# Kernel tuning notes

Hardware: AMD Instinct MI355X
Metric: run time of the kernel (lower is better)

The kernel has to match this reference:

```python
import jax, jax.numpy as jnp
import numpy as np

B, N, C, H, NC = 8, 4096, 512, 256, 1000
GRID = 64  # N = GRID*GRID unique positions
LN_EPS = 1e-5


def setup_inputs() -> dict:
    key = jax.random.key(0)
    ks = jax.random.split(key, 10)
    # unique integer grid positions, same for every batch element (original order)
    i = jnp.arange(N)
    base = jnp.stack([i % GRID, i // GRID], axis=-1).astype(jnp.float32)  # [N,2]
    pos_org = jnp.broadcast_to(base, (B, N, 2))
    # per-batch random permutation -> shuffled positions (as the backbone would emit)
    perm = jax.vmap(lambda k: jax.random.permutation(k, N))(jax.random.split(ks[0], B))  # [B,N]
    pos_shuffled = jnp.take_along_axis(pos_org, perm[..., None], axis=1)
    s = 0.02
    return {
        "feat": jax.random.normal(ks[1], (B, N, C), jnp.float32),
        "prev_out": jax.random.normal(ks[2], (B, N, C), jnp.float32),
        "pos_org": pos_org,
        "pos_shuffled": pos_shuffled,
        "proj_W": jax.random.normal(ks[3], (C, C), jnp.float32) * s,
        "proj_b": jnp.zeros((C,), jnp.float32),
        "ln_g": jnp.ones((C,), jnp.float32),
        "ln_b": jnp.zeros((C,), jnp.float32),
        "W1": jax.random.normal(ks[4], (H, C), jnp.float32) * s,
        "b1": jnp.zeros((H,), jnp.float32),
        "W2": jax.random.normal(ks[5], (H, H), jnp.float32) * s,
        "b2": jnp.zeros((H,), jnp.float32),
        "W3": jax.random.normal(ks[6], (NC, H), jnp.float32) * s,
        "b3": jnp.zeros((NC,), jnp.float32),
    }


def _layernorm(x, g, b):
    x32 = x.astype(jnp.float32)
    mu = x32.mean(-1, keepdims=True)
    var = ((x32 - mu) ** 2).mean(-1, keepdims=True)
    return (x32 - mu) * jax.lax.rsqrt(var + LN_EPS) * g + b


def reference(feat, prev_out, pos_org, pos_shuffled, proj_W, proj_b,
              ln_g, ln_b, W1, b1, W2, b2, W3, b3):
    # find_pos_org_order: L1 cdist [B,N,N] + argmin over shuffled axis
    dists = jnp.abs(pos_org[:, :, None, :] - pos_shuffled[:, None, :, :]).sum(-1)
    pos_indices = jnp.argmin(dists, axis=2)  # [B,N]
    # batched gather: feat[b_, pos_indices]
    g = jnp.take_along_axis(feat, pos_indices[..., None], axis=1)  # [B,N,C]
    # fused proj -> layernorm (in fp32) -> cast back -> residual add
    proj = jnp.einsum('bnc,dc->bnd', g, proj_W) + proj_b
    out_feat = prev_out + _layernorm(proj, ln_g, ln_b).astype(feat.dtype)
    # mean-pool over tokens, 3-layer MLP head with relu on first two layers
    pooled = out_feat.mean(1)  # [B,C]
    h = jax.nn.relu(pooled @ W1.T + b1)
    h = jax.nn.relu(h @ W2.T + b2)
    return h @ W3.T + b3  # [B, num_classes]
```

## Files before the change

kernel.cpp:

```cpp
#include <hip/hip_runtime.h>
#include <stdint.h>

#define B_ 8
#define N_ 4096
#define C_ 512
#define H_ 256
#define NC_ 1000

typedef float v4f __attribute__((ext_vector_type(4)));
typedef short v8s __attribute__((ext_vector_type(8)));
typedef unsigned short ushort_t;

__device__ __forceinline__ uint32_t f2bf1(float f) {
    uint32_t u = __float_as_uint(f);
    return (u + 0x7FFFu + ((u >> 16) & 1u)) >> 16;
}
__device__ __forceinline__ uint32_t pk2(float lo, float hi) {
#if __has_builtin(__builtin_amdgcn_cvt_pk_bf16_f32)
    auto r = __builtin_amdgcn_cvt_pk_bf16_f32(lo, hi);
    return __builtin_bit_cast(uint32_t, r);
#else
    return f2bf1(lo) | (f2bf1(hi) << 16);
#endif
}

__global__ void prep_kernel(const float* __restrict__ W, ushort_t* __restrict__ Wfrag) {
    int i = blockIdx.x * 256 + threadIdx.x;
    int d = i >> 6, kb = (i >> 2) & 15, q = i & 3;
    const float4* src = (const float4*)(W + d * C_ + kb * 32 + q * 8);
    float4 v0 = src[0], v1 = src[1];
    uint4 pk;
    pk.x = pk2(v0.x, v0.y); pk.y = pk2(v0.z, v0.w);
    pk.z = pk2(v1.x, v1.y); pk.w = pk2(v1.z, v1.w);
    ((uint4*)Wfrag)[((d >> 4) * 16 + kb) * 64 + q * 16 + (d & 15)] = pk;
}

__device__ __forceinline__ void kstep(int kb, v4f (&acc)[4][4],
                                      const ushort_t* const (&fb)[4],
                                      const v8s* __restrict__ Abuf,
                                      int c, int q) {
    v8s af[4], bf[4];
#pragma unroll
    for (int nt = 0; nt < 4; nt++)
        bf[nt] = *((const v8s*)(fb[nt] + kb * 512));
#pragma unroll
    for (int mt = 0; mt < 4; mt++)
        af[mt] = Abuf[(mt * 16 + c) * 64 + ((kb * 4 + q) ^ (c & 7))];
#pragma unroll
    for (int mt = 0; mt < 4; mt++)
#pragma unroll
        for (int nt = 0; nt < 4; nt++)
            acc[mt][nt] = __builtin_amdgcn_mfma_f32_16x16x32_bf16(
                af[mt], bf[nt], acc[mt][nt], 0, 0, 0);
}

__global__ __launch_bounds__(512, 4)
void gemm_ln_pool(const float* __restrict__ feat, const float* __restrict__ prev,
                  const ushort_t* __restrict__ Wfrag,
                  const float* __restrict__ pb, const float* __restrict__ lg,
                  const float* __restrict__ lb,
                  float* __restrict__ partialG,
                  float* __restrict__ partialP) {
    __shared__ v8s Abuf[4096];
    __shared__ float RowS[64], RowQ[64];

    const int bid = blockIdx.x;
    const int t = threadIdx.x;

    if (bid % 3 == 2) {
        const int p = bid / 3;
        const int b = p >> 5;
        const int r0 = (p & 31) << 7;
        const int col4 = t & 127, rg = t >> 7;
        const v4f* psrc =
            (const v4f*)(prev + (size_t)(b * N_ + r0 + rg * 32) * C_) + col4;
        v4f a0 = {0.f, 0.f, 0.f, 0.f}, a1 = a0, a2 = a0, a3 = a0;
#pragma unroll
        for (int batch = 0; batch < 4; batch++) {
            v4f v[8];
#pragma unroll
            for (int j = 0; j < 8; j++)
                v[j] = __builtin_nontemporal_load(psrc + (batch * 8 + j) * 128);
            a0 += v[0]; a1 += v[1]; a2 += v[2]; a3 += v[3];
            a0 += v[4]; a1 += v[5]; a2 += v[6]; a3 += v[7];
        }
        v4f s = (a0 + a1) + (a2 + a3);
        float* AbufF = (float*)Abuf;
        ((v4f*)AbufF)[rg * 128 + col4] = s;
        __syncthreads();
        partialP[(size_t)p * 512 + t] =
            (AbufF[t] + AbufF[512 + t]) + (AbufF[1024 + t] + AbufF[1536 + t]);
        return;
    }

    const int gix = (bid / 3) * 2 + (bid % 3);
    const int b = gix >> 6;
    const int row0 = (gix & 63) << 6;
    const int wv = t >> 6, lane = t & 63, c = lane & 15, q = lane >> 4;

    if (t < 64) { RowS[t] = 0.f; RowQ[t] = 0.f; }

    const int arow = t >> 3;
    const int acol8 = t & 7;
    const v4f* asrc = (const v4f*)(feat + ((size_t)(b * N_ + row0 + arow) * C_));
#pragma unroll 2
    for (int s = 0; s < 4; s++) {
        const int chunk = s * 8 + acol8;
        v4f f0 = __builtin_nontemporal_load(asrc + chunk * 2);
        v4f f1 = __builtin_nontemporal_load(asrc + chunk * 2 + 1);
        uint4 pk;
        pk.x = pk2(f0.x, f0.y); pk.y = pk2(f0.z, f0.w);
        pk.z = pk2(f1.x, f1.y); pk.w = pk2(f1.z, f1.w);
        ((uint4*)Abuf)[arow * 64 + (chunk ^ (arow & 7))] = pk;
    }

    const ushort_t* fb[4];
#pragma unroll
    for (int nt = 0; nt < 4; nt++)
        fb[nt] = Wfrag + (wv * 4 + nt) * 8192 + lane * 8;

    v4f acc[4][4];
    const v4f vzero = {0.f, 0.f, 0.f, 0.f};
#pragma unroll
    for (int mt = 0; mt < 4; mt++)
#pragma unroll
        for (int nt = 0; nt < 4; nt++) acc[mt][nt] = vzero;

    __syncthreads();

#pragma unroll 2
    for (int kb = 0; kb < 6; kb++) kstep(kb, acc, fb, Abuf, c, q);

#pragma unroll 2
    for (int s = 4; s < 8; s++) {
        const int chunk = s * 8 + acol8;
        v4f f0 = __builtin_nontemporal_load(asrc + chunk * 2);
        v4f f1 = __builtin_nontemporal_load(asrc + chunk * 2 + 1);
        uint4 pk;
        pk.x = pk2(f0.x, f0.y); pk.y = pk2(f0.z, f0.w);
        pk.z = pk2(f1.x, f1.y); pk.w = pk2(f1.z, f1.w);
        ((uint4*)Abuf)[arow * 64 + (chunk ^ (arow & 7))] = pk;
    }

    kstep(6, acc, fb, Abuf, c, q);
    kstep(7, acc, fb, Abuf, c, q);
    __syncthreads();

#pragma unroll 2
    for (int kb = 8; kb < 16; kb++) kstep(kb, acc, fb, Abuf, c, q);

    float pb4[4], lg4[4], lb4[4];
#pragma unroll
    for (int nt = 0; nt < 4; nt++) {
        int n = wv * 64 + nt * 16 + c;
        pb4[nt] = pb[n]; lg4[nt] = lg[n]; lb4[nt] = lb[n];
    }
#pragma unroll
    for (int mt = 0; mt < 4; mt++) {
#pragma unroll
        for (int reg = 0; reg < 4; reg++) {
            float s1 = 0.f, s2 = 0.f;
#pragma unroll
            for (int nt = 0; nt < 4; nt++) {
                float v = acc[mt][nt][reg] + pb4[nt];
                acc[mt][nt][reg] = v;
                s1 += v; s2 += v * v;
            }
#pragma unroll
            for (int d = 1; d < 16; d <<= 1) {
                s1 += __shfl_xor(s1, d);
                s2 += __shfl_xor(s2, d);
            }
            if (c == 0) {
                int r = mt * 16 + q * 4 + reg;
                atomicAdd(&RowS[r], s1);
                atomicAdd(&RowQ[r], s2);
            }
        }
    }
    __syncthreads();
    if (t < 64) {
        float mu = RowS[t] * (1.f / C_);
        float var = RowQ[t] * (1.f / C_) - mu * mu;
        RowS[t] = mu;
        RowQ[t] = rsqrtf(var + 1e-5f);
    }
    __syncthreads();
    float col[4] = {0.f, 0.f, 0.f, 0.f};
#pragma unroll
    for (int mt = 0; mt < 4; mt++) {
#pragma unroll
        for (int reg = 0; reg < 4; reg++) {
            int r = mt * 16 + q * 4 + reg;
            float mu = RowS[r], rs = RowQ[r];
#pragma unroll
            for (int nt = 0; nt < 4; nt++)
                col[nt] += (acc[mt][nt][reg] - mu) * rs * lg4[nt] + lb4[nt];
        }
    }
#pragma unroll
    for (int nt = 0; nt < 4; nt++) {
        col[nt] += __shfl_xor(col[nt], 16);
        col[nt] += __shfl_xor(col[nt], 32);
    }
    if (lane < 16) {
#pragma unroll
        for (int nt = 0; nt < 4; nt++)
            partialG[(size_t)gix * 512 + wv * 64 + nt * 16 + c] = col[nt];
    }
}

__global__ __launch_bounds__(256)
void head_kernel(const float* __restrict__ partialG,
                 const float* __restrict__ partialP,
                 const float* __restrict__ W1, const float* __restrict__ b1,
                 const float* __restrict__ W2, const float* __restrict__ b2,
                 const float* __restrict__ W3, const float* __restrict__ b3,
                 float* __restrict__ out) {
    __shared__ __align__(16) float P[512];
    __shared__ __align__(16) float H1[256];
    __shared__ __align__(16) float H2[256];
    const int t = threadIdx.x, wv = t >> 6, lane = t & 63;
    const int b = blockIdx.x / 25;
    const int slice = blockIdx.x % 25;

    {
        const float* pg = partialG + (size_t)b * 64 * 512;
        const float* pp = partialP + (size_t)b * 32 * 512;
        float a0 = 0.f, a1 = 0.f, a2 = 0.f, a3 = 0.f;
#pragma unroll 4
        for (int i = 0; i < 64; i += 2) {
            a0 += pg[i * 512 + t];
            a1 += pg[(i + 1) * 512 + t];
            a2 += pg[i * 512 + t + 256];
            a3 += pg[(i + 1) * 512 + t + 256];
        }
#pragma unroll 4
        for (int i = 0; i < 32; i += 2) {
            a0 += pp[i * 512 + t];
            a1 += pp[(i + 1) * 512 + t];
            a2 += pp[i * 512 + t + 256];
            a3 += pp[(i + 1) * 512 + t + 256];
        }
        P[t] = (a0 + a1) * (1.f / 4096.f);
        P[t + 256] = (a2 + a3) * (1.f / 4096.f);
    }
    __syncthreads();

    {
        const float4* wr = (const float4*)(W1 + t * C_);
        float s = 0.f;
#pragma unroll 8
        for (int k = 0; k < 128; k++) {
            float4 w = wr[k];
            float4 p = ((const float4*)P)[k];
            s += w.x * p.x + w.y * p.y + w.z * p.z + w.w * p.w;
        }
        H1[t] = fmaxf(s + b1[t], 0.f);
    }
    __syncthreads();

    {
        const float4* wr = (const float4*)(W2 + t * H_);
        float s = 0.f;
#pragma unroll 8
        for (int k = 0; k < 64; k++) {
            float4 w = wr[k];
            float4 p = ((const float4*)H1)[k];
            s += w.x * p.x + w.y * p.y + w.z * p.z + w.w * p.w;
        }
        H2[t] = fmaxf(s + b2[t], 0.f);
    }
    __syncthreads();

#pragma unroll
    for (int jj = 0; jj < 10; jj++) {
        const int o = slice * 40 + jj * 4 + wv;
        float4 w = ((const float4*)(W3 + o * H_))[lane];
        float4 p = ((const float4*)H2)[lane];
        float s = w.x * p.x + w.y * p.y + w.z * p.z + w.w * p.w;
#pragma unroll
        for (int d = 1; d < 64; d <<= 1) s += __shfl_xor(s, d);
        if (lane == 0) out[b * NC_ + o] = s + b3[o];
    }
}

extern "C" void kernel_launch(void* const* d_in, const int* in_sizes, int n_in,
                              void* d_out, int out_size, void* d_ws, size_t ws_size,
                              hipStream_t stream) {
    const float* feat  = (const float*)d_in[0];
    const float* prev  = (const float*)d_in[1];
    const float* projW = (const float*)d_in[4];
    const float* pb    = (const float*)d_in[5];
    const float* lg    = (const float*)d_in[6];
    const float* lb    = (const float*)d_in[7];
    const float* W1    = (const float*)d_in[8];
    const float* b1    = (const float*)d_in[9];
    const float* W2    = (const float*)d_in[10];
    const float* b2    = (const float*)d_in[11];
    const float* W3    = (const float*)d_in[12];
    const float* b3    = (const float*)d_in[13];
    float* out = (float*)d_out;

    char* ws = (char*)d_ws;
    ushort_t* Wfrag  = (ushort_t*)ws;
    float* partialG  = (float*)(ws + 524288);
    float* partialP  = (float*)(ws + 1572864);

    prep_kernel<<<128, 256, 0, stream>>>(projW, Wfrag);
    gemm_ln_pool<<<768, 512, 0, stream>>>(feat, prev, Wfrag,
                                          pb, lg, lb, partialG, partialP);
    head_kernel<<<200, 256, 0, stream>>>(partialG, partialP,
                                         W1, b1, W2, b2, W3, b3, out);
}
```

Measured before the change: 222.3 us.

## Fuse MLP head into GEMM kernel via last-block-per-batch atomic counter

Drops the separate head kernel launch. Each block of the GEMM/pool kernel bumps a per-batch atomic counter after writing its partials, and the last of the 96 blocks for that batch reduces the partials and runs the three-layer MLP. This removes a kernel launch and its gap, but the head now runs on only 8 blocks instead of 200. Each thread also computes a whole 256-long W3 row serially, which could lengthen the tail.

```diff
diff --git a/kernel.cpp b/kernel.cpp
--- a/kernel.cpp
+++ b/kernel.cpp
@@ -24,8 +24,11 @@
 #endif
 }
 
-__global__ void prep_kernel(const float* __restrict__ W, ushort_t* __restrict__ Wfrag) {
-    int i = blockIdx.x * 256 + threadIdx.x;
+__global__ void prep_kernel(const float* __restrict__ W, ushort_t* __restrict__ Wfrag,
+                            uint32_t* __restrict__ counters) {
+    int t = threadIdx.x;
+    if (blockIdx.x == 0 && t < 8) counters[t] = 0;
+    int i = blockIdx.x * 256 + t;
     int d = i >> 6, kb = (i >> 2) & 15, q = i & 3;
     const float4* src = (const float4*)(W + d * C_ + kb * 32 + q * 8);
     float4 v0 = src[0], v1 = src[1];
@@ -60,16 +63,23 @@
                   const float* __restrict__ pb, const float* __restrict__ lg,
                   const float* __restrict__ lb,
                   float* __restrict__ partialG,
-                  float* __restrict__ partialP) {
+                  float* __restrict__ partialP,
+                  uint32_t* __restrict__ counters,
+                  const float* __restrict__ W1, const float* __restrict__ b1,
+                  const float* __restrict__ W2, const float* __restrict__ b2,
+                  const float* __restrict__ W3, const float* __restrict__ b3,
+                  float* __restrict__ out) {
     __shared__ v8s Abuf[4096];
     __shared__ float RowS[64], RowQ[64];
+    __shared__ int isLast;
 
     const int bid = blockIdx.x;
     const int t = threadIdx.x;
+    int b;
 
     if (bid % 3 == 2) {
         const int p = bid / 3;
-        const int b = p >> 5;
+        b = p >> 5;
         const int r0 = (p & 31) << 7;
         const int col4 = t & 127, rg = t >> 7;
         const v4f* psrc =
@@ -90,198 +100,196 @@
         __syncthreads();
         partialP[(size_t)p * 512 + t] =
             (AbufF[t] + AbufF[512 + t]) + (AbufF[1024 + t] + AbufF[1536 + t]);
-        return;
-    }
-
-    const int gix = (bid / 3) * 2 + (bid % 3);
-    const int b = gix >> 6;
-    const int row0 = (gix & 63) << 6;
-    const int wv = t >> 6, lane = t & 63, c = lane & 15, q = lane >> 4;
-
-    if (t < 64) { RowS[t] = 0.f; RowQ[t] = 0.f; }
-
-    const int arow = t >> 3;
-    const int acol8 = t & 7;
-    const v4f* asrc = (const v4f*)(feat + ((size_t)(b * N_ + row0 + arow) * C_));
+    } else {
+        const int gix = (bid / 3) * 2 + (bid % 3);
+        b = gix >> 6;
+        const int row0 = (gix & 63) << 6;
+        const int wv = t >> 6, lane = t & 63, c = lane & 15, q = lane >> 4;
+
+        if (t < 64) { RowS[t] = 0.f; RowQ[t] = 0.f; }
+
+        const int arow = t >> 3;
+        const int acol8 = t & 7;
+        const v4f* asrc = (const v4f*)(feat + ((size_t)(b * N_ + row0 + arow) * C_));
 #pragma unroll 2
-    for (int s = 0; s < 4; s++) {
-        const int chunk = s * 8 + acol8;
-        v4f f0 = __builtin_nontemporal_load(asrc + chunk * 2);
-        v4f f1 = __builtin_nontemporal_load(asrc + chunk * 2 + 1);
-        uint4 pk;
-        pk.x = pk2(f0.x, f0.y); pk.y = pk2(f0.z, f0.w);
-        pk.z = pk2(f1.x, f1.y); pk.w = pk2(f1.z, f1.w);
-        ((uint4*)Abuf)[arow * 64 + (chunk ^ (arow & 7))] = pk;
-    }
-
-    const ushort_t* fb[4];
-#pragma unroll
-    for (int nt = 0; nt < 4; nt++)
-        fb[nt] = Wfrag + (wv * 4 + nt) * 8192 + lane * 8;
-
-    v4f acc[4][4];
-    const v4f vzero = {0.f, 0.f, 0.f, 0.f};
-#pragma unroll
-    for (int mt = 0; mt < 4; mt++)
-#pragma unroll
-        for (int nt = 0; nt < 4; nt++) acc[mt][nt] = vzero;
-
-    __syncthreads();
+        for (int s = 0; s < 4; s++) {
+            const int chunk = s * 8 + acol8;
+            v4f f0 = __builtin_nontemporal_load(asrc + chunk * 2);
+            v4f f1 = __builtin_nontemporal_load(asrc + chunk * 2 + 1);
+            uint4 pk;
+            pk.x = pk2(f0.x, f0.y); pk.y = pk2(f0.z, f0.w);
+            pk.z = pk2(f1.x, f1.y); pk.w = pk2(f1.z, f1.w);
+            ((uint4*)Abuf)[arow * 64 + (chunk ^ (arow & 7))] = pk;
+        }
+
+        const ushort_t* fb[4];
+#pragma unroll
+        for (int nt = 0; nt < 4; nt++)
+            fb[nt] = Wfrag + (wv * 4 + nt) * 8192 + lane * 8;
+
+        v4f acc[4][4];
+        const v4f vzero = {0.f, 0.f, 0.f, 0.f};
+#pragma unroll
+        for (int mt = 0; mt < 4; mt++)
+#pragma unroll
+            for (int nt = 0; nt < 4; nt++) acc[mt][nt] = vzero;
+
+        __syncthreads();
 
 #pragma unroll 2
-    for (int kb = 0; kb < 6; kb++) kstep(kb, acc, fb, Abuf, c, q);
+        for (int kb = 0; kb < 6; kb++) kstep(kb, acc, fb, Abuf, c, q);
 
 #pragma unroll 2
-    for (int s = 4; s < 8; s++) {
-        const int chunk = s * 8 + acol8;
-        v4f f0 = __builtin_nontemporal_load(asrc + chunk * 2);
-        v4f f1 = __builtin_nontemporal_load(asrc + chunk * 2 + 1);
-        uint4 pk;
-        pk.x = pk2(f0.x, f0.y); pk.y = pk2(f0.z, f0.w);
-        pk.z = pk2(f1.x, f1.y); pk.w = pk2(f1.z, f1.w);
-        ((uint4*)Abuf)[arow * 64 + (chunk ^ (arow & 7))] = pk;
-    }
-
-    kstep(6, acc, fb, Abuf, c, q);
-    kstep(7, acc, fb, Abuf, c, q);
-    __syncthreads();
+        for (int s = 4; s < 8; s++) {
+            const int chunk = s * 8 + acol8;
+            v4f f0 = __builtin_nontemporal_load(asrc + chunk * 2);
+            v4f f1 = __builtin_nontemporal_load(asrc + chunk * 2 + 1);
+            uint4 pk;
+            pk.x = pk2(f0.x, f0.y); pk.y = pk2(f0.z, f0.w);
+            pk.z = pk2(f1.x, f1.y); pk.w = pk2(f1.z, f1.w);
+            ((uint4*)Abuf)[arow * 64 + (chunk ^ (arow & 7))] = pk;
+        }
+
+        kstep(6, acc, fb, Abuf, c, q);
+        kstep(7, acc, fb, Abuf, c, q);
+        __syncthreads();
 
 #pragma unroll 2
-    for (int kb = 8; kb < 16; kb++) kstep(kb, acc, fb, Abuf, c, q);
-
-    float pb4[4], lg4[4], lb4[4];
-#pragma unroll
-    for (int nt = 0; nt < 4; nt++) {
-        int n = wv * 64 + nt * 16 + c;
-        pb4[nt] = pb[n]; lg4[nt] = lg[n]; lb4[nt] = lb[n];
-    }
-#pragma unroll
-    for (int mt = 0; mt < 4; mt++) {
-#pragma unroll
-        for (int reg = 0; reg < 4; reg++) {
-            float s1 = 0.f, s2 = 0.f;
-#pragma unroll
-            for (int nt = 0; nt < 4; nt++) {
-                float v = acc[mt][nt][reg] + pb4[nt];
-                acc[mt][nt][reg] = v;
-                s1 += v; s2 += v * v;
+        for (int kb = 8; kb < 16; kb++) kstep(kb, acc, fb, Abuf, c, q);
+
+        float pb4[4], lg4[4], lb4[4];
+#pragma unroll
+        for (int nt = 0; nt < 4; nt++) {
+            int n = wv * 64 + nt * 16 + c;
+            pb4[nt] = pb[n]; lg4[nt] = lg[n]; lb4[nt] = lb[n];
+        }
+#pragma unroll
+        for (int mt = 0; mt < 4; mt++) {
+#pragma unroll
+            for (int reg = 0; reg < 4; reg++) {
+                float s1 = 0.f, s2 = 0.f;
+#pragma unroll
+                for (int nt = 0; nt < 4; nt++) {
+                    float v = acc[mt][nt][reg] + pb4[nt];
+                    acc[mt][nt][reg] = v;
+                    s1 += v; s2 += v * v;
+                }
+#pragma unroll
+                for (int d = 1; d < 16; d <<= 1) {
+                    s1 += __shfl_xor(s1, d);
+                    s2 += __shfl_xor(s2, d);
+                }
+                if (c == 0) {
+                    int r = mt * 16 + q * 4 + reg;
+                    atomicAdd(&RowS[r], s1);
+                    atomicAdd(&RowQ[r], s2);
+                }
             }
-#pragma unroll
-            for (int d = 1; d < 16; d <<= 1) {
-                s1 += __shfl_xor(s1, d);
-                s2 += __shfl_xor(s2, d);
+        }
+        __syncthreads();
+        if (t < 64) {
+            float mu = RowS[t] * (1.f / C_);
+            float var = RowQ[t] * (1.f / C_) - mu * mu;
+            RowS[t] = mu;
+            RowQ[t] = rsqrtf(var + 1e-5f);
+        }
+        __syncthreads();
+        float col[4] = {0.f, 0.f, 0.f, 0.f};
+#pragma unroll
+        for (int mt = 0; mt < 4; mt++) {
+#pragma unroll
+            for (int reg = 0; reg < 4; reg++) {
+                int r = mt * 16 + q * 4 + reg;
+                float mu = RowS[r], rs = RowQ[r];
+#pragma unroll
+                for (int nt = 0; nt < 4; nt++)
+                    col[nt] += (acc[mt][nt][reg] - mu) * rs * lg4[nt] + lb4[nt];
             }
-            if (c == 0) {
-                int r = mt * 16 + q * 4 + reg;
-                atomicAdd(&RowS[r], s1);
-                atomicAdd(&RowQ[r], s2);
-            }
-        }
-    }
-    __syncthreads();
-    if (t < 64) {
-        float mu = RowS[t] * (1.f / C_);
-        float var = RowQ[t] * (1.f / C_) - mu * mu;
-        RowS[t] = mu;
-        RowQ[t] = rsqrtf(var + 1e-5f);
-    }
-    __syncthreads();
-    float col[4] = {0.f, 0.f, 0.f, 0.f};
-#pragma unroll
-    for (int mt = 0; mt < 4; mt++) {
-#pragma unroll
-        for (int reg = 0; reg < 4; reg++) {
-            int r = mt * 16 + q * 4 + reg;
-            float mu = RowS[r], rs = RowQ[r];
+        }
+#pragma unroll
+        for (int nt = 0; nt < 4; nt++) {
+            col[nt] += __shfl_xor(col[nt], 16);
+            col[nt] += __shfl_xor(col[nt], 32);
+        }
+        if (lane < 16) {
 #pragma unroll
             for (int nt = 0; nt < 4; nt++)
-                col[nt] += (acc[mt][nt][reg] - mu) * rs * lg4[nt] + lb4[nt];
-        }
-    }
-#pragma unroll
-    for (int nt = 0; nt < 4; nt++) {
-        col[nt] += __shfl_xor(col[nt], 16);
-        col[nt] += __shfl_xor(col[nt], 32);
-    }
-    if (lane < 16) {
-#pragma unroll
-        for (int nt = 0; nt < 4; nt++)
-            partialG[(size_t)gix * 512 + wv * 64 + nt * 16 + c] = col[nt];
-    }
-}
-
-__global__ __launch_bounds__(256)
-void head_kernel(const float* __restrict__ partialG,
-                 const float* __restrict__ partialP,
-                 const float* __restrict__ W1, const float* __restrict__ b1,
-                 const float* __restrict__ W2, const float* __restrict__ b2,
-                 const float* __restrict__ W3, const float* __restrict__ b3,
-                 float* __restrict__ out) {
-    __shared__ __align__(16) float P[512];
-    __shared__ __align__(16) float H1[256];
-    __shared__ __align__(16) float H2[256];
-    const int t = threadIdx.x, wv = t >> 6, lane = t & 63;
-    const int b = blockIdx.x / 25;
-    const int slice = blockIdx.x % 25;
-
+                partialG[(size_t)gix * 512 + wv * 64 + nt * 16 + c] = col[nt];
+        }
+    }
+
+    __threadfence();
+    __syncthreads();
+    if (t == 0) {
+        uint32_t prev_cnt = atomicAdd(&counters[b], 1u);
+        isLast = (prev_cnt == 95u);
+    }
+    __syncthreads();
+    if (!isLast) return;
+    __threadfence();
+
+    float* P  = (float*)Abuf;
+    float* H1 = P + 512;
+    float* H2 = H1 + 256;
     {
-        const float* pg = partialG + (size_t)b * 64 * 512;
-        const float* pp = partialP + (size_t)b * 32 * 512;
+        const float* pg = partialG + (size_t)b * 64 * 512 + t;
+        const float* pp = partialP + (size_t)b * 32 * 512 + t;
         float a0 = 0.f, a1 = 0.f, a2 = 0.f, a3 = 0.f;
 #pragma unroll 4
-        for (int i = 0; i < 64; i += 2) {
-            a0 += pg[i * 512 + t];
-            a1 += pg[(i + 1) * 512 + t];
-            a2 += pg[i * 512 + t + 256];
-            a3 += pg[(i + 1) * 512 + t + 256];
+        for (int i = 0; i < 64; i += 4) {
+            a0 += pg[(i + 0) * 512]; a1 += pg[(i + 1) * 512];
+            a2 += pg[(i + 2) * 512]; a3 += pg[(i + 3) * 512];
         }
 #pragma unroll 4
-        for (int i = 0; i < 32; i += 2) {
-            a0 += pp[i * 512 + t];
-            a1 += pp[(i + 1) * 512 + t];
-            a2 += pp[i * 512 + t + 256];
-            a3 += pp[(i + 1) * 512 + t + 256];
-        }
-        P[t] = (a0 + a1) * (1.f / 4096.f);
-        P[t + 256] = (a2 + a3) * (1.f / 4096.f);
+        for (int i = 0; i < 32; i += 4) {
+            a0 += pp[(i + 0) * 512]; a1 += pp[(i + 1) * 512];
+            a2 += pp[(i + 2) * 512]; a3 += pp[(i + 3) * 512];
+        }
+        P[t] = ((a0 + a1) + (a2 + a3)) * (1.f / 4096.f);
     }
     __syncthreads();
 
     {
-        const float4* wr = (const float4*)(W1 + t * C_);
         float s = 0.f;
+        if (t < 256) {
+            const float4* wr = (const float4*)(W1 + t * C_);
 #pragma unroll 8
-        for (int k = 0; k < 128; k++) {
-            float4 w = wr[k];
-            float4 p = ((const float4*)P)[k];
-            s += w.x * p.x + w.y * p.y + w.z * p.z + w.w * p.w;
-        }
-        H1[t] = fmaxf(s + b1[t], 0.f);
+            for (int k = 0; k < 128; k++) {
+                float4 w = wr[k];
+                float4 p = ((const float4*)P)[k];
+                s += w.x * p.x + w.y * p.y + w.z * p.z + w.w * p.w;
+            }
+        }
+        __syncthreads();
+        if (t < 256) H1[t] = fmaxf(s + b1[t], 0.f);
     }
     __syncthreads();
 
     {
-        const float4* wr = (const float4*)(W2 + t * H_);
+        float s = 0.f;
+        if (t < 256) {
+            const float4* wr = (const float4*)(W2 + t * H_);
+#pragma unroll 8
+            for (int k = 0; k < 64; k++) {
+                float4 w = wr[k];
+                float4 p = ((const float4*)H1)[k];
+                s += w.x * p.x + w.y * p.y + w.z * p.z + w.w * p.w;
+            }
+            H2[t] = fmaxf(s + b2[t], 0.f);
+        }
+    }
+    __syncthreads();
+
+    for (int o = t; o < NC_; o += 512) {
+        const float4* wr = (const float4*)(W3 + o * H_);
         float s = 0.f;
 #pragma unroll 8
         for (int k = 0; k < 64; k++) {
             float4 w = wr[k];
-            float4 p = ((const float4*)H1)[k];
+            float4 p = ((const float4*)H2)[k];
             s += w.x * p.x + w.y * p.y + w.z * p.z + w.w * p.w;
         }
-        H2[t] = fmaxf(s + b2[t], 0.f);
-    }
-    __syncthreads();
-
-#pragma unroll
-    for (int jj = 0; jj < 10; jj++) {
-        const int o = slice * 40 + jj * 4 + wv;
-        float4 w = ((const float4*)(W3 + o * H_))[lane];
-        float4 p = ((const float4*)H2)[lane];
-        float s = w.x * p.x + w.y * p.y + w.z * p.z + w.w * p.w;
-#pragma unroll
-        for (int d = 1; d < 64; d <<= 1) s += __shfl_xor(s, d);
-        if (lane == 0) out[b * NC_ + o] = s + b3[o];
+        out[b * NC_ + o] = s + b3[o];
     }
 }
 
@@ -303,13 +311,13 @@
     float* out = (float*)d_out;
 
     char* ws = (char*)d_ws;
-    ushort_t* Wfrag  = (ushort_t*)ws;
-    float* partialG  = (float*)(ws + 524288);
-    float* partialP  = (float*)(ws + 1572864);
-
-    prep_kernel<<<128, 256, 0, stream>>>(projW, Wfrag);
-    gemm_ln_pool<<<768, 512, 0, stream>>>(feat, prev, Wfrag,
-                                          pb, lg, lb, partialG, partialP);
-    head_kernel<<<200, 256, 0, stream>>>(partialG, partialP,
-                                         W1, b1, W2, b2, W3, b3, out);
-}
+    ushort_t* Wfrag    = (ushort_t*)ws;
+    float* partialG    = (float*)(ws + 524288);
+    float* partialP    = (float*)(ws + 1572864);
+    uint32_t* counters = (uint32_t*)(ws + 2097152);
+
+    prep_kernel<<<128, 256, 0, stream>>>(projW, Wfrag, counters);
+    gemm_ln_pool<<<768, 512, 0, stream>>>(feat, prev, Wfrag, pb, lg, lb,
+                                          partialG, partialP, counters,
+                                          W1, b1, W2, b2, W3, b3, out);
+}
```

Result: slower. 511.2 us (+130.0%).
